# Performance work log

Measured on AMD Instinct MI355X. Metric: run time of the kernel, lower is better.

## Reference

```python
import jax, jax.numpy as jnp
import numpy as np

B, IN, H, OUT = 1024, 512, 1024, 512   # tokens, input, hidden (MoE width), output
E, K, LAYERS = 8, 2, 10                 # experts, top-k, repeated MoE applications
EPS = 1e-10
LOSS_COEF = 0.01


def setup_inputs() -> dict:
    key = jax.random.key(0)
    ks = jax.random.split(key, 8)
    s = 0.02  # small init scale for weights
    return {
        "x": jax.random.normal(ks[0], (B, IN), jnp.float32),
        "enc_w": jax.random.normal(ks[1], (IN, H), jnp.float32) * s,
        "enc_b": jnp.zeros((H,), jnp.float32),
        "w_gate": jax.random.normal(ks[2], (H, E), jnp.float32) * s,
        "w1": jax.random.normal(ks[3], (E, H, H), jnp.float32) * s,
        "b1": jnp.zeros((E, H), jnp.float32),
        "w2": jax.random.normal(ks[4], (E, H, H), jnp.float32) * s,
        "b2": jnp.zeros((E, H), jnp.float32),
        "dec_w": jax.random.normal(ks[5], (H, OUT), jnp.float32) * s,
        "dec_b": jnp.zeros((OUT,), jnp.float32),
    }


def _cv_squared(v):
    # torch .var() is unbiased (ddof=1)
    return jnp.var(v, ddof=1) / (jnp.mean(v) ** 2 + EPS)


def _moe_layer(h, w_gate, w1, b1, w2, b2):
    # top-k gating (eval / no-noise path of noisy_top_k_gating)
    logits = h @ w_gate                                  # [B, E]
    top_vals, top_idx = jax.lax.top_k(logits, K)         # [B, K]
    gk = jax.nn.softmax(top_vals, axis=-1)               # softmax over top-k logits
    b = h.shape[0]
    gates = jnp.zeros((b, E), h.dtype).at[jnp.arange(b)[:, None], top_idx].set(gk)
    importance = gates.sum(axis=0)                       # [E]
    load = (gates > 0).sum(axis=0).astype(h.dtype)       # [E]
    aux = LOSS_COEF * (_cv_squared(importance) + _cv_squared(load))
    # experts: Linear -> ReLU -> Linear; combine weighted by gates
    # (dense-over-experts form; math identical to sparse dispatch/combine)
    hid = jax.nn.relu(jnp.einsum('bh,ehf->bef', h, w1) + b1)  # [B, E, H]
    y = jnp.einsum('bef,efo->beo', hid, w2) + b2              # [B, E, H]
    out = jnp.einsum('be,beo->bo', gates, y)                  # [B, H]
    return out, aux


def reference(x, enc_w, enc_b, w_gate, w1, b1, w2, b2, dec_w, dec_b):
    h = jax.nn.relu(x @ enc_w + enc_b)
    loss = jnp.zeros((), h.dtype)
    for _ in range(LAYERS):  # same MoE module (shared params) applied 10 times
        h, aux = _moe_layer(h, w_gate, w1, b1, w2, b2)
        loss = loss + aux
    out = jax.nn.relu(h @ dec_w + dec_b)
    return out, loss
```

## Files before the change

### kernel.cpp

```cpp
#include <hip/hip_runtime.h>
#include <math.h>

#define TPB 256
typedef unsigned short u16;
typedef unsigned int u32;
typedef __bf16 bf16x8 __attribute__((ext_vector_type(8)));
typedef float f32x4 __attribute__((ext_vector_type(4)));

namespace {
constexpr int NTOK  = 1024;
constexpr int IND   = 512;
constexpr int HD    = 1024;
constexpr int OUTD  = 512;
constexpr int NE    = 8;
constexpr int NSLOT = 2048;
}

__device__ __forceinline__ u16 f2bf(float f) {
  u32 x = __float_as_uint(f);
  x += 0x7fffu + ((x >> 16) & 1u);
  return (u16)(x >> 16);
}
__device__ __forceinline__ float bf2f(u16 u) { return __uint_as_float(((u32)u) << 16); }
__device__ __forceinline__ void split2(float v, u16& h, u16& l) {
  h = f2bf(v);
  l = f2bf(v - bf2f(h));
}

__device__ __forceinline__ void gll16(const void* g, void* l) {
  __builtin_amdgcn_global_load_lds((const __attribute__((address_space(1))) void*)g,
                                   (__attribute__((address_space(3))) void*)l, 16, 0, 0);
}


__global__ __launch_bounds__(TPB)
void transpose_split(const float* __restrict__ in, u16* __restrict__ ohi,
                     u16* __restrict__ olo, int K, int N)
{
  const int z = blockIdx.z;
  in  += (size_t)z * K * N;
  ohi += (size_t)z * K * N;
  olo += (size_t)z * K * N;
  __shared__ float tile[32][33];
  const int k0 = blockIdx.y * 32, n0 = blockIdx.x * 32;
  const int tx = threadIdx.x & 31, ty = threadIdx.x >> 5;
#pragma unroll
  for (int i = 0; i < 4; ++i) {
    int k = ty + i * 8;
    tile[k][tx] = in[(size_t)(k0 + k) * N + n0 + tx];
  }
  __syncthreads();
#pragma unroll
  for (int i = 0; i < 4; ++i) {
    int n = ty + i * 8;
    float v = tile[tx][n];
    u16 h, l; split2(v, h, l);
    size_t o = (size_t)(n0 + n) * K + k0 + tx;
    ohi[o] = h; olo[o] = l;
  }
}

__global__ __launch_bounds__(TPB)
void split_rows(const float* __restrict__ in, u16* __restrict__ oh,
                u16* __restrict__ ol, int nelem)
{
  int i = blockIdx.x * TPB + threadIdx.x;
  if (i * 4 >= nelem) return;
  float4 v = ((const float4*)in)[i];
  ushort4 H, L;
  split2(v.x, H.x, L.x); split2(v.y, H.y, L.y);
  split2(v.z, H.z, L.z); split2(v.w, H.w, L.w);
  ((ushort4*)oh)[i] = H;
  ((ushort4*)ol)[i] = L;
}

template<bool RELU, bool GROUPED, bool GATHER, bool SPLIT_OUT>
__global__ __launch_bounds__(TPB)
void gemm_split(const u16* __restrict__ Ah, const u16* __restrict__ Al,
                const int* __restrict__ gatherIdx,
                const u16* __restrict__ Bh, const u16* __restrict__ Bl,
                const float* __restrict__ bias,
                float* __restrict__ Cf, u16* __restrict__ Ch, u16* __restrict__ Cl,
                const int* __restrict__ seg_off, const int* __restrict__ seg_cnt,
                int M, int K, int N)
{
  const int e = GROUPED ? blockIdx.z : 0;
  int cnt = M, base = 0;
  if (GROUPED) { cnt = seg_cnt[e]; base = seg_off[e]; }
  const int tm = blockIdx.y, tn = blockIdx.x;
  if (tm * 64 >= cnt) return;

  __shared__ u16 smem[24576];
  constexpr int AHo = 0, ALo = 4096, BHo = 8192, BLo = 16384;

  const int t = threadIdx.x;
  const int wid = t >> 6, lane = t & 63;
  const int wr = wid >> 1, wc = wid & 1;

  const u16* aph[2]; const u16* apl[2];
#pragma unroll
  for (int i = 0; i < 2; ++i) {
    int slot = t + i * TPB;
    int row = slot >> 3, kblk = slot & 7;
    int kbs = kblk ^ (row & 7);
    int row_in = tm * 64 + row;
    int rv = row_in < cnt ? row_in : 0;
    int src;
    if (GATHER)      src = gatherIdx[base + rv];
    else             src = GROUPED ? base + rv : rv;
    size_t off = (size_t)src * K + kbs * 8;
    aph[i] = Ah + off; apl[i] = Al + off;
  }
  const u16* bph[4]; const u16* bpl[4];
  const size_t bbase = GROUPED ? (size_t)e * N * K : 0;
#pragma unroll
  for (int i = 0; i < 4; ++i) {
    int slot = t + i * TPB;
    int n = slot >> 3, kblk = slot & 7;
    int kbs = kblk ^ (n & 7);
    size_t off = bbase + (size_t)(tn * 128 + n) * K + kbs * 8;
    bph[i] = Bh + off; bpl[i] = Bl + off;
  }

  f32x4 acc[2][4];
#pragma unroll
  for (int i = 0; i < 2; ++i)
#pragma unroll
    for (int j = 0; j < 4; ++j) acc[i][j] = (f32x4){0.f, 0.f, 0.f, 0.f};

  for (int k0 = 0; k0 < K; k0 += 64) {
#pragma unroll
    for (int i = 0; i < 2; ++i) {
      int ldso = (wid * 64 + i * TPB) * 8;
      gll16(aph[i] + k0, &smem[AHo + ldso]);
      gll16(apl[i] + k0, &smem[ALo + ldso]);
    }
#pragma unroll
    for (int i = 0; i < 4; ++i) {
      int ldso = (wid * 64 + i * TPB) * 8;
      gll16(bph[i] + k0, &smem[BHo + ldso]);
      gll16(bpl[i] + k0, &smem[BLo + ldso]);
    }
    __syncthreads();

#pragma unroll
    for (int s = 0; s < 2; ++s) {
      const int kb = s * 4 + (lane >> 4);
      bf16x8 fah[2], fal[2];
#pragma unroll
      for (int fr = 0; fr < 2; ++fr) {
        int ar = wr * 32 + fr * 16 + (lane & 15);
        int off = ar * 64 + ((kb ^ (ar & 7)) << 3);
        fah[fr] = *(const bf16x8*)&smem[AHo + off];
        fal[fr] = *(const bf16x8*)&smem[ALo + off];
      }
      bf16x8 fbh[4], fbl[4];
#pragma unroll
      for (int fc = 0; fc < 4; ++fc) {
        int bn = wc * 64 + fc * 16 + (lane & 15);
        int off = bn * 64 + ((kb ^ (bn & 7)) << 3);
        fbh[fc] = *(const bf16x8*)&smem[BHo + off];
        fbl[fc] = *(const bf16x8*)&smem[BLo + off];
      }
#pragma unroll
      for (int fr = 0; fr < 2; ++fr)
#pragma unroll
        for (int fc = 0; fc < 4; ++fc) {
          acc[fr][fc] = __builtin_amdgcn_mfma_f32_16x16x32_bf16(fah[fr], fbh[fc], acc[fr][fc], 0, 0, 0);
          acc[fr][fc] = __builtin_amdgcn_mfma_f32_16x16x32_bf16(fah[fr], fbl[fc], acc[fr][fc], 0, 0, 0);
          acc[fr][fc] = __builtin_amdgcn_mfma_f32_16x16x32_bf16(fal[fr], fbh[fc], acc[fr][fc], 0, 0, 0);
        }
    }
    __syncthreads();
  }

  const float* bp = bias + (GROUPED ? (size_t)e * N : 0);
#pragma unroll
  for (int fr = 0; fr < 2; ++fr) {
#pragma unroll
    for (int q = 0; q < 4; ++q) {
      int row_in = tm * 64 + wr * 32 + fr * 16 + ((lane >> 4) << 2) + q;
      if (row_in >= cnt) continue;
      size_t orow = (size_t)(GROUPED ? base + row_in : row_in);
#pragma unroll
      for (int fc = 0; fc < 4; ++fc) {
        int col = tn * 128 + wc * 64 + fc * 16 + (lane & 15);
        float v = acc[fr][fc][q] + bp[col];
        if (RELU) v = fmaxf(v, 0.f);
        if (SPLIT_OUT) {
          u16 h, l; split2(v, h, l);
          Ch[orow * N + col] = h;
          Cl[orow * N + col] = l;
        } else {
          Cf[orow * N + col] = v;
        }
      }
    }
  }
}

__global__ __launch_bounds__(TPB)
void gate_split(const u16* __restrict__ hh, const u16* __restrict__ hl,
                const float* __restrict__ w_gate,
                int* __restrict__ eidx, float* __restrict__ gval)
{
  const int b = blockIdx.x, t = threadIdx.x;
  float acc[NE] = {};
  for (int i = t; i < HD; i += TPB) {
    float hv = bf2f(hh[(size_t)b * HD + i]) + bf2f(hl[(size_t)b * HD + i]);
    const float* wg = w_gate + (size_t)i * NE;
#pragma unroll
    for (int e = 0; e < NE; ++e) acc[e] = fmaf(hv, wg[e], acc[e]);
  }
  __shared__ float red[TPB][NE];
#pragma unroll
  for (int e = 0; e < NE; ++e) red[t][e] = acc[e];
  __syncthreads();
  for (int s = TPB / 2; s > 0; s >>= 1) {
    if (t < s) {
#pragma unroll
      for (int e = 0; e < NE; ++e) red[t][e] += red[t + s][e];
    }
    __syncthreads();
  }
  if (t == 0) {
    float v1 = -1e30f; int e1 = 0;
#pragma unroll
    for (int e = 0; e < NE; ++e) { float v = red[0][e]; if (v > v1) { v1 = v; e1 = e; } }
    float v2 = -1e30f; int e2 = 0;
#pragma unroll
    for (int e = 0; e < NE; ++e) {
      if (e == e1) continue;
      float v = red[0][e]; if (v > v2) { v2 = v; e2 = e; }
    }
    float ev = expf(v2 - v1);
    eidx[b * 2] = e1;  eidx[b * 2 + 1] = e2;
    gval[b * 2] = 1.f / (1.f + ev);  gval[b * 2 + 1] = ev / (1.f + ev);
  }
}

__global__ __launch_bounds__(TPB)
void stats_scatter(const int* __restrict__ eidx, const float* __restrict__ gval,
                   float* __restrict__ loss, int* __restrict__ seg_off,
                   int* __restrict__ seg_cnt, int* __restrict__ slot_token,
                   int* __restrict__ slot_of)
{
  const int t = threadIdx.x;
  float imp[NE] = {};
  int   cnt[NE] = {};
  for (int s = t; s < NSLOT; s += TPB) {
    int e = eidx[s]; float g = gval[s];
#pragma unroll
    for (int q = 0; q < NE; ++q) if (q == e) { imp[q] += g; cnt[q]++; }
  }
  __shared__ float rimp[TPB][NE];
  __shared__ int   rcnt[TPB][NE];
#pragma unroll
  for (int e = 0; e < NE; ++e) { rimp[t][e] = imp[e]; rcnt[t][e] = cnt[e]; }
  __syncthreads();
  for (int s = TPB / 2; s > 0; s >>= 1) {
    if (t < s) {
#pragma unroll
      for (int e = 0; e < NE; ++e) { rimp[t][e] += rimp[t + s][e]; rcnt[t][e] += rcnt[t + s][e]; }
    }
    __syncthreads();
  }
  __shared__ int s_off[NE], s_fill[NE];
  if (t == 0) {
    float mi = 0.f, ml = 0.f;
#pragma unroll
    for (int e = 0; e < NE; ++e) { mi += rimp[0][e]; ml += (float)rcnt[0][e]; }
    mi /= NE; ml /= NE;
    float vi = 0.f, vl = 0.f;
#pragma unroll
    for (int e = 0; e < NE; ++e) {
      float di = rimp[0][e] - mi; vi += di * di;
      float dl = (float)rcnt[0][e] - ml; vl += dl * dl;
    }
    vi /= (NE - 1); vl /= (NE - 1);
    loss[0] += 0.01f * (vi / (mi * mi + 1e-10f) + vl / (ml * ml + 1e-10f));
    int off = 0;
#pragma unroll
    for (int e = 0; e < NE; ++e) {
      seg_off[e] = off; seg_cnt[e] = rcnt[0][e];
      s_off[e] = off; s_fill[e] = 0; off += rcnt[0][e];
    }
  }
  __syncthreads();
  for (int s = t; s < NSLOT; s += TPB) {
    int e = eidx[s];
    int pos = s_off[e] + atomicAdd(&s_fill[e], 1);
    slot_token[pos] = s >> 1;
    slot_of[s] = pos;
  }
}

__global__ __launch_bounds__(TPB)
void combine_split(const float* __restrict__ y, const float* __restrict__ gval,
                   const int* __restrict__ slot_of,
                   u16* __restrict__ hh, u16* __restrict__ hl)
{
  const int b = blockIdx.x, t = threadIdx.x;
  const int p0 = slot_of[b * 2], p1 = slot_of[b * 2 + 1];
  const float g0 = gval[b * 2], g1 = gval[b * 2 + 1];
  const float4* y0 = (const float4*)(y + (size_t)p0 * HD);
  const float4* y1 = (const float4*)(y + (size_t)p1 * HD);
  for (int i = t; i < HD / 4; i += TPB) {
    float4 a = y0[i], c = y1[i];
    float v0 = g0 * a.x + g1 * c.x, v1 = g0 * a.y + g1 * c.y;
    float v2 = g0 * a.z + g1 * c.z, v3 = g0 * a.w + g1 * c.w;
    ushort4 H, L;
    split2(v0, H.x, L.x); split2(v1, H.y, L.y);
    split2(v2, H.z, L.z); split2(v3, H.w, L.w);
    ((ushort4*)hh)[(size_t)b * (HD / 4) + i] = H;
    ((ushort4*)hl)[(size_t)b * (HD / 4) + i] = L;
  }
}

__global__ void init_kernel(float* loss) { loss[0] = 0.f; }
__global__ void write_loss(const float* __restrict__ loss, float* __restrict__ out)
{ out[0] = loss[0]; }

template<bool RELU, bool GROUPED, bool GATHER>
__global__ __launch_bounds__(TPB)
void gemm_f32(const float* __restrict__ A, const int* __restrict__ gatherIdx,
              const float* __restrict__ B, const float* __restrict__ bias,
              float* __restrict__ C, const int* __restrict__ seg_off,
              const int* __restrict__ seg_cnt, int M, int K, int N)
{
  const int e = GROUPED ? blockIdx.z : 0;
  int cnt = M, base = 0;
  if (GROUPED) { cnt = seg_cnt[e]; base = seg_off[e]; }
  const int tm = blockIdx.y, tn = blockIdx.x;
  if (tm * 64 >= cnt) return;
  const float* Bp = B + (size_t)e * K * N;
  const float* bp = bias + (size_t)e * N;
  __shared__ float As[16][68];
  __shared__ float Bs[16][64];
  const int t = threadIdx.x;
  const int rm0 = (t >> 4) << 2, cn0 = (t & 15) << 2;
  int arow[4]; bool aval[4];
#pragma unroll
  for (int i = 0; i < 4; ++i) {
    int idx = t + i * TPB;
    int r = idx >> 4;
    int row_in = tm * 64 + r;
    bool v = row_in < cnt;
    int src;
    if (GATHER) src = v ? gatherIdx[base + row_in] : 0;
    else        src = v ? (GROUPED ? base + row_in : row_in) : 0;
    arow[i] = src; aval[i] = v;
  }
  float acc[4][4] = {};
  for (int k0 = 0; k0 < K; k0 += 16) {
#pragma unroll
    for (int i = 0; i < 4; ++i) {
      int idx = t + i * TPB;
      int r = idx >> 4, kk = idx & 15;
      As[kk][r] = aval[i] ? A[(size_t)arow[i] * K + k0 + kk] : 0.f;
    }
#pragma unroll
    for (int i = 0; i < 4; ++i) {
      int idx = t + i * TPB;
      int kk = idx >> 6, n = idx & 63;
      Bs[kk][n] = Bp[(size_t)(k0 + kk) * N + tn * 64 + n];
    }
    __syncthreads();
#pragma unroll
    for (int kk = 0; kk < 16; ++kk) {
      const float4 a4 = *(const float4*)&As[kk][rm0];
      const float4 b4 = *(const float4*)&Bs[kk][cn0];
      float av[4] = {a4.x, a4.y, a4.z, a4.w};
      float bv[4] = {b4.x, b4.y, b4.z, b4.w};
#pragma unroll
      for (int i = 0; i < 4; ++i)
#pragma unroll
        for (int j = 0; j < 4; ++j) acc[i][j] = fmaf(av[i], bv[j], acc[i][j]);
    }
    __syncthreads();
  }
#pragma unroll
  for (int i = 0; i < 4; ++i) {
    int row_in = tm * 64 + rm0 + i;
    if (row_in >= cnt) continue;
    size_t orow = (size_t)(base + row_in);
    float v0 = acc[i][0] + bp[tn * 64 + cn0 + 0];
    float v1 = acc[i][1] + bp[tn * 64 + cn0 + 1];
    float v2 = acc[i][2] + bp[tn * 64 + cn0 + 2];
    float v3 = acc[i][3] + bp[tn * 64 + cn0 + 3];
    if (RELU) { v0 = fmaxf(v0, 0.f); v1 = fmaxf(v1, 0.f); v2 = fmaxf(v2, 0.f); v3 = fmaxf(v3, 0.f); }
    *(float4*)&C[orow * N + tn * 64 + cn0] = make_float4(v0, v1, v2, v3);
  }
}

__global__ __launch_bounds__(TPB)
void gate_f32(const float* __restrict__ h, const float* __restrict__ w_gate,
              int* __restrict__ eidx, float* __restrict__ gval)
{
  const int b = blockIdx.x, t = threadIdx.x;
  float acc[NE] = {};
  const float* hb = h + (size_t)b * HD;
  for (int i = t; i < HD; i += TPB) {
    float hv = hb[i];
    const float* wg = w_gate + (size_t)i * NE;
#pragma unroll
    for (int e = 0; e < NE; ++e) acc[e] = fmaf(hv, wg[e], acc[e]);
  }
  __shared__ float red[TPB][NE];
#pragma unroll
  for (int e = 0; e < NE; ++e) red[t][e] = acc[e];
  __syncthreads();
  for (int s = TPB / 2; s > 0; s >>= 1) {
    if (t < s) {
#pragma unroll
      for (int e = 0; e < NE; ++e) red[t][e] += red[t + s][e];
    }
    __syncthreads();
  }
  if (t == 0) {
    float v1 = -1e30f; int e1 = 0;
#pragma unroll
    for (int e = 0; e < NE; ++e) { float v = red[0][e]; if (v > v1) { v1 = v; e1 = e; } }
    float v2 = -1e30f; int e2 = 0;
#pragma unroll
    for (int e = 0; e < NE; ++e) {
      if (e == e1) continue;
      float v = red[0][e]; if (v > v2) { v2 = v; e2 = e; }
    }
    float ev = expf(v2 - v1);
    eidx[b * 2] = e1;  eidx[b * 2 + 1] = e2;
    gval[b * 2] = 1.f / (1.f + ev);  gval[b * 2 + 1] = ev / (1.f + ev);
  }
}

__global__ __launch_bounds__(TPB)
void combine_f32(const float* __restrict__ y, const float* __restrict__ gval,
                 const int* __restrict__ slot_of, float* __restrict__ h)
{
  const int b = blockIdx.x, t = threadIdx.x;
  const int p0 = slot_of[b * 2], p1 = slot_of[b * 2 + 1];
  const float g0 = gval[b * 2], g1 = gval[b * 2 + 1];
  const float4* y0 = (const float4*)(y + (size_t)p0 * HD);
  const float4* y1 = (const float4*)(y + (size_t)p1 * HD);
  float4* hb = (float4*)(h + (size_t)b * HD);
  for (int i = t; i < HD / 4; i += TPB) {
    float4 a = y0[i], c = y1[i];
    hb[i] = make_float4(g0 * a.x + g1 * c.x, g0 * a.y + g1 * c.y,
                        g0 * a.z + g1 * c.z, g0 * a.w + g1 * c.w);
  }
}


extern "C" void kernel_launch(void* const* d_in, const int* in_sizes, int n_in,
                              void* d_out, int out_size, void* d_ws, size_t ws_size,
                              hipStream_t stream)
{
  const float* x      = (const float*)d_in[0];
  const float* enc_w  = (const float*)d_in[1];
  const float* enc_b  = (const float*)d_in[2];
  const float* w_gate = (const float*)d_in[3];
  const float* w1     = (const float*)d_in[4];
  const float* b1     = (const float*)d_in[5];
  const float* w2     = (const float*)d_in[6];
  const float* b2     = (const float*)d_in[7];
  const float* dec_w  = (const float*)d_in[8];
  const float* dec_b  = (const float*)d_in[9];
  float* outp = (float*)d_out;
  dim3 blk(TPB);

  const size_t NEED = 100ull << 20;
  if (ws_size >= NEED) {
    char* p = (char*)d_ws;
    auto alloc = [&](size_t bytes) { char* r = p; p += (bytes + 255) & ~(size_t)255; return r; };
    u16* w1t_h = (u16*)alloc((size_t)NE * HD * HD * 2);
    u16* w1t_l = (u16*)alloc((size_t)NE * HD * HD * 2);
    u16* w2t_h = (u16*)alloc((size_t)NE * HD * HD * 2);
    u16* w2t_l = (u16*)alloc((size_t)NE * HD * HD * 2);
    u16* ewt_h = (u16*)alloc((size_t)IND * HD * 2);
    u16* ewt_l = (u16*)alloc((size_t)IND * HD * 2);
    u16* dwt_h = (u16*)alloc((size_t)HD * OUTD * 2);
    u16* dwt_l = (u16*)alloc((size_t)HD * OUTD * 2);
    u16* x_h   = (u16*)alloc((size_t)NTOK * IND * 2);
    u16* x_l   = (u16*)alloc((size_t)NTOK * IND * 2);
    u16* h_h   = (u16*)alloc((size_t)NTOK * HD * 2);
    u16* h_l   = (u16*)alloc((size_t)NTOK * HD * 2);
    u16* hid_h = (u16*)alloc((size_t)NSLOT * HD * 2);
    u16* hid_l = (u16*)alloc((size_t)NSLOT * HD * 2);
    float* y   = (float*)alloc((size_t)NSLOT * HD * 4);
    int*   eidx       = (int*)alloc(NSLOT * 4);
    float* gval       = (float*)alloc(NSLOT * 4);
    int*   slot_of    = (int*)alloc(NSLOT * 4);
    int*   slot_token = (int*)alloc(NSLOT * 4);
    int*   seg_off    = (int*)alloc(256);
    int*   seg_cnt    = (int*)alloc(256);
    float* loss       = (float*)alloc(256);

    init_kernel<<<1, 1, 0, stream>>>(loss);
    transpose_split<<<dim3(HD / 32, HD / 32, NE), blk, 0, stream>>>(w1, w1t_h, w1t_l, HD, HD);
    transpose_split<<<dim3(HD / 32, HD / 32, NE), blk, 0, stream>>>(w2, w2t_h, w2t_l, HD, HD);
    transpose_split<<<dim3(HD / 32, IND / 32, 1), blk, 0, stream>>>(enc_w, ewt_h, ewt_l, IND, HD);
    transpose_split<<<dim3(OUTD / 32, HD / 32, 1), blk, 0, stream>>>(dec_w, dwt_h, dwt_l, HD, OUTD);
    split_rows<<<(NTOK * IND / 4 + TPB - 1) / TPB, blk, 0, stream>>>(x, x_h, x_l, NTOK * IND);

    gemm_split<true, false, false, true><<<dim3(HD / 128, NTOK / 64, 1), blk, 0, stream>>>(
        x_h, x_l, nullptr, ewt_h, ewt_l, enc_b, nullptr, h_h, h_l, nullptr, nullptr,
        NTOK, IND, HD);

    for (int L = 0; L < 10; ++L) {
      gate_split<<<NTOK, blk, 0, stream>>>(h_h, h_l, w_gate, eidx, gval);
      stats_scatter<<<1, blk, 0, stream>>>(eidx, gval, loss, seg_off, seg_cnt,
                                           slot_token, slot_of);
      gemm_split<true, true, true, true><<<dim3(HD / 128, NSLOT / 64, NE), blk, 0, stream>>>(
          h_h, h_l, slot_token, w1t_h, w1t_l, b1, nullptr, hid_h, hid_l,
          seg_off, seg_cnt, 0, HD, HD);
      gemm_split<false, true, false, false><<<dim3(HD / 128, NSLOT / 64, NE), blk, 0, stream>>>(
          hid_h, hid_l, nullptr, w2t_h, w2t_l, b2, y, nullptr, nullptr,
          seg_off, seg_cnt, 0, HD, HD);
      combine_split<<<NTOK, blk, 0, stream>>>(y, gval, slot_of, h_h, h_l);
    }

    gemm_split<true, false, false, false><<<dim3(OUTD / 128, NTOK / 64, 1), blk, 0, stream>>>(
        h_h, h_l, nullptr, dwt_h, dwt_l, dec_b, outp, nullptr, nullptr, nullptr, nullptr,
        NTOK, HD, OUTD);
    write_loss<<<1, 1, 0, stream>>>(loss, outp + NTOK * OUTD);
    return;
  }

  char* ws = (char*)d_ws;
  float* h   = (float*)(ws);
  float* hid = (float*)(ws + (4u  << 20));
  float* y   = (float*)(ws + (12u << 20));
  char* sp = ws + (20u << 20);
  int*   eidx       = (int*)sp;    sp += NSLOT * 4;
  float* gval       = (float*)sp;  sp += NSLOT * 4;
  int*   slot_of    = (int*)sp;    sp += NSLOT * 4;
  int*   slot_token = (int*)sp;    sp += NSLOT * 4;
  int*   seg_off    = (int*)sp;    sp += 64;
  int*   seg_cnt    = (int*)sp;    sp += 64;
  float* loss       = (float*)sp;  sp += 64;

  init_kernel<<<1, 1, 0, stream>>>(loss);
  gemm_f32<true, false, false><<<dim3(HD / 64, NTOK / 64, 1), blk, 0, stream>>>(
      x, nullptr, enc_w, enc_b, h, nullptr, nullptr, NTOK, IND, HD);
  for (int L = 0; L < 10; ++L) {
    gate_f32<<<NTOK, blk, 0, stream>>>(h, w_gate, eidx, gval);
    stats_scatter<<<1, blk, 0, stream>>>(eidx, gval, loss, seg_off, seg_cnt,
                                         slot_token, slot_of);
    gemm_f32<true, true, true><<<dim3(HD / 64, NTOK / 64, NE), blk, 0, stream>>>(
        h, slot_token, w1, b1, hid, seg_off, seg_cnt, 0, HD, HD);
    gemm_f32<false, true, false><<<dim3(HD / 64, NTOK / 64, NE), blk, 0, stream>>>(
        hid, nullptr, w2, b2, y, seg_off, seg_cnt, 0, HD, HD);
    combine_f32<<<NTOK, blk, 0, stream>>>(y, gval, slot_of, h);
  }
  gemm_f32<true, false, false><<<dim3(OUTD / 64, NTOK / 64, 1), blk, 0, stream>>>(
      h, nullptr, dec_w, dec_b, outp, nullptr, nullptr, NTOK, HD, OUTD);
  write_loss<<<1, 1, 0, stream>>>(loss, outp + NTOK * OUTD);
}
```

Baseline: 945.5 us.

## Double-buffer split-bf16 GEMM tiles and fuse gating into the combine kernel

The split-bf16 MFMA GEMM now double-buffers its LDS tiles, issuing global-to-LDS loads for the next K step while computing on the current one. This is meant to hide load latency behind the MFMA work, at the cost of doubling shared memory per block to 96 KB, which can cut the number of resident blocks per CU. The gate kernel now reads its inputs with vector loads. The per-layer gate launch is also folded into the combine kernel, which computes the top-2 gating for the next layer from the freshly combined activations, saving one launch per layer and one re-read of the hidden state.

```diff
diff --git a/kernel.cpp b/kernel.cpp
--- a/kernel.cpp
+++ b/kernel.cpp
@@ -90,8 +90,8 @@
   const int tm = blockIdx.y, tn = blockIdx.x;
   if (tm * 64 >= cnt) return;
 
-  __shared__ u16 smem[24576];
-  constexpr int AHo = 0, ALo = 4096, BHo = 8192, BLo = 16384;
+  __shared__ u16 smem[49152];
+  constexpr int AHo = 0, ALo = 4096, BHo = 8192, BLo = 16384, BUF = 24576;
 
   const int t = threadIdx.x;
   const int wid = t >> 6, lane = t & 63;
@@ -122,27 +122,28 @@
     bph[i] = Bh + off; bpl[i] = Bl + off;
   }
 
-  f32x4 acc[2][4];
-#pragma unroll
-  for (int i = 0; i < 2; ++i)
-#pragma unroll
-    for (int j = 0; j < 4; ++j) acc[i][j] = (f32x4){0.f, 0.f, 0.f, 0.f};
-
-  for (int k0 = 0; k0 < K; k0 += 64) {
+  auto stage = [&](int bb, int k0) {
 #pragma unroll
     for (int i = 0; i < 2; ++i) {
       int ldso = (wid * 64 + i * TPB) * 8;
-      gll16(aph[i] + k0, &smem[AHo + ldso]);
-      gll16(apl[i] + k0, &smem[ALo + ldso]);
+      gll16(aph[i] + k0, &smem[bb + AHo + ldso]);
+      gll16(apl[i] + k0, &smem[bb + ALo + ldso]);
     }
 #pragma unroll
     for (int i = 0; i < 4; ++i) {
       int ldso = (wid * 64 + i * TPB) * 8;
-      gll16(bph[i] + k0, &smem[BHo + ldso]);
-      gll16(bpl[i] + k0, &smem[BLo + ldso]);
-    }
-    __syncthreads();
-
+      gll16(bph[i] + k0, &smem[bb + BHo + ldso]);
+      gll16(bpl[i] + k0, &smem[bb + BLo + ldso]);
+    }
+  };
+
+  f32x4 acc[2][4];
+#pragma unroll
+  for (int i = 0; i < 2; ++i)
+#pragma unroll
+    for (int j = 0; j < 4; ++j) acc[i][j] = (f32x4){0.f, 0.f, 0.f, 0.f};
+
+  auto compute = [&](int bb) {
 #pragma unroll
     for (int s = 0; s < 2; ++s) {
       const int kb = s * 4 + (lane >> 4);
@@ -150,7 +151,7 @@
 #pragma unroll
       for (int fr = 0; fr < 2; ++fr) {
         int ar = wr * 32 + fr * 16 + (lane & 15);
-        int off = ar * 64 + ((kb ^ (ar & 7)) << 3);
+        int off = bb + ar * 64 + ((kb ^ (ar & 7)) << 3);
         fah[fr] = *(const bf16x8*)&smem[AHo + off];
         fal[fr] = *(const bf16x8*)&smem[ALo + off];
       }
@@ -158,7 +159,7 @@
 #pragma unroll
       for (int fc = 0; fc < 4; ++fc) {
         int bn = wc * 64 + fc * 16 + (lane & 15);
-        int off = bn * 64 + ((kb ^ (bn & 7)) << 3);
+        int off = bb + bn * 64 + ((kb ^ (bn & 7)) << 3);
         fbh[fc] = *(const bf16x8*)&smem[BHo + off];
         fbl[fc] = *(const bf16x8*)&smem[BLo + off];
       }
@@ -171,8 +172,18 @@
           acc[fr][fc] = __builtin_amdgcn_mfma_f32_16x16x32_bf16(fal[fr], fbh[fc], acc[fr][fc], 0, 0, 0);
         }
     }
+  };
+
+  stage(0, 0);
+  int cur = 0;
+  for (int k0 = 64; k0 < K; k0 += 64) {
     __syncthreads();
-  }
+    stage((cur ^ 1) * BUF, k0);
+    compute(cur * BUF);
+    cur ^= 1;
+  }
+  __syncthreads();
+  compute(cur * BUF);
 
   const float* bp = bias + (GROUPED ? (size_t)e * N : 0);
 #pragma unroll
@@ -205,12 +216,20 @@
                 int* __restrict__ eidx, float* __restrict__ gval)
 {
   const int b = blockIdx.x, t = threadIdx.x;
+  ushort4 H = ((const ushort4*)(hh + (size_t)b * HD))[t];
+  ushort4 L = ((const ushort4*)(hl + (size_t)b * HD))[t];
+  float hv[4] = { bf2f(H.x) + bf2f(L.x), bf2f(H.y) + bf2f(L.y),
+                  bf2f(H.z) + bf2f(L.z), bf2f(H.w) + bf2f(L.w) };
   float acc[NE] = {};
-  for (int i = t; i < HD; i += TPB) {
-    float hv = bf2f(hh[(size_t)b * HD + i]) + bf2f(hl[(size_t)b * HD + i]);
-    const float* wg = w_gate + (size_t)i * NE;
-#pragma unroll
-    for (int e = 0; e < NE; ++e) acc[e] = fmaf(hv, wg[e], acc[e]);
+  const int i0 = t * 4;
+#pragma unroll
+  for (int j = 0; j < 4; ++j) {
+    const float4* wg = (const float4*)(w_gate + (size_t)(i0 + j) * NE);
+    float4 w0 = wg[0], w1 = wg[1];
+    acc[0] = fmaf(hv[j], w0.x, acc[0]); acc[1] = fmaf(hv[j], w0.y, acc[1]);
+    acc[2] = fmaf(hv[j], w0.z, acc[2]); acc[3] = fmaf(hv[j], w0.w, acc[3]);
+    acc[4] = fmaf(hv[j], w1.x, acc[4]); acc[5] = fmaf(hv[j], w1.y, acc[5]);
+    acc[6] = fmaf(hv[j], w1.z, acc[6]); acc[7] = fmaf(hv[j], w1.w, acc[7]);
   }
   __shared__ float red[TPB][NE];
 #pragma unroll
@@ -295,25 +314,63 @@
   }
 }
 
-__global__ __launch_bounds__(TPB)
-void combine_split(const float* __restrict__ y, const float* __restrict__ gval,
-                   const int* __restrict__ slot_of,
-                   u16* __restrict__ hh, u16* __restrict__ hl)
+template<bool GATE>
+__global__ __launch_bounds__(TPB)
+void combine_gate(const float* __restrict__ y, const float* __restrict__ gv_in,
+                  const int* __restrict__ slot_of, const float* __restrict__ w_gate,
+                  u16* __restrict__ hh, u16* __restrict__ hl,
+                  int* __restrict__ eidx, float* __restrict__ gval)
 {
   const int b = blockIdx.x, t = threadIdx.x;
   const int p0 = slot_of[b * 2], p1 = slot_of[b * 2 + 1];
-  const float g0 = gval[b * 2], g1 = gval[b * 2 + 1];
-  const float4* y0 = (const float4*)(y + (size_t)p0 * HD);
-  const float4* y1 = (const float4*)(y + (size_t)p1 * HD);
-  for (int i = t; i < HD / 4; i += TPB) {
-    float4 a = y0[i], c = y1[i];
-    float v0 = g0 * a.x + g1 * c.x, v1 = g0 * a.y + g1 * c.y;
-    float v2 = g0 * a.z + g1 * c.z, v3 = g0 * a.w + g1 * c.w;
-    ushort4 H, L;
-    split2(v0, H.x, L.x); split2(v1, H.y, L.y);
-    split2(v2, H.z, L.z); split2(v3, H.w, L.w);
-    ((ushort4*)hh)[(size_t)b * (HD / 4) + i] = H;
-    ((ushort4*)hl)[(size_t)b * (HD / 4) + i] = L;
+  const float g0 = gv_in[b * 2], g1 = gv_in[b * 2 + 1];
+  float4 a = ((const float4*)(y + (size_t)p0 * HD))[t];
+  float4 c = ((const float4*)(y + (size_t)p1 * HD))[t];
+  float v[4] = { g0 * a.x + g1 * c.x, g0 * a.y + g1 * c.y,
+                 g0 * a.z + g1 * c.z, g0 * a.w + g1 * c.w };
+  ushort4 H, L;
+  split2(v[0], H.x, L.x); split2(v[1], H.y, L.y);
+  split2(v[2], H.z, L.z); split2(v[3], H.w, L.w);
+  ((ushort4*)(hh + (size_t)b * HD))[t] = H;
+  ((ushort4*)(hl + (size_t)b * HD))[t] = L;
+
+  if (GATE) {
+    float acc[NE] = {};
+    const int i0 = t * 4;
+#pragma unroll
+    for (int j = 0; j < 4; ++j) {
+      const float4* wg = (const float4*)(w_gate + (size_t)(i0 + j) * NE);
+      float4 w0 = wg[0], w1 = wg[1];
+      acc[0] = fmaf(v[j], w0.x, acc[0]); acc[1] = fmaf(v[j], w0.y, acc[1]);
+      acc[2] = fmaf(v[j], w0.z, acc[2]); acc[3] = fmaf(v[j], w0.w, acc[3]);
+      acc[4] = fmaf(v[j], w1.x, acc[4]); acc[5] = fmaf(v[j], w1.y, acc[5]);
+      acc[6] = fmaf(v[j], w1.z, acc[6]); acc[7] = fmaf(v[j], w1.w, acc[7]);
+    }
+    __shared__ float red[TPB][NE];
+#pragma unroll
+    for (int e = 0; e < NE; ++e) red[t][e] = acc[e];
+    __syncthreads();
+    for (int s = TPB / 2; s > 0; s >>= 1) {
+      if (t < s) {
+#pragma unroll
+        for (int e = 0; e < NE; ++e) red[t][e] += red[t + s][e];
+      }
+      __syncthreads();
+    }
+    if (t == 0) {
+      float v1 = -1e30f; int e1 = 0;
+#pragma unroll
+      for (int e = 0; e < NE; ++e) { float vv = red[0][e]; if (vv > v1) { v1 = vv; e1 = e; } }
+      float v2 = -1e30f; int e2 = 0;
+#pragma unroll
+      for (int e = 0; e < NE; ++e) {
+        if (e == e1) continue;
+        float vv = red[0][e]; if (vv > v2) { v2 = vv; e2 = e; }
+      }
+      float ev = expf(v2 - v1);
+      eidx[b * 2] = e1;  eidx[b * 2 + 1] = e2;
+      gval[b * 2] = 1.f / (1.f + ev);  gval[b * 2 + 1] = ev / (1.f + ev);
+    }
   }
 }
 
@@ -506,8 +563,8 @@
         x_h, x_l, nullptr, ewt_h, ewt_l, enc_b, nullptr, h_h, h_l, nullptr, nullptr,
         NTOK, IND, HD);
 
+    gate_split<<<NTOK, blk, 0, stream>>>(h_h, h_l, w_gate, eidx, gval);
     for (int L = 0; L < 10; ++L) {
-      gate_split<<<NTOK, blk, 0, stream>>>(h_h, h_l, w_gate, eidx, gval);
       stats_scatter<<<1, blk, 0, stream>>>(eidx, gval, loss, seg_off, seg_cnt,
                                            slot_token, slot_of);
       gemm_split<true, true, true, true><<<dim3(HD / 128, NSLOT / 64, NE), blk, 0, stream>>>(
@@ -516,7 +573,12 @@
       gemm_split<false, true, false, false><<<dim3(HD / 128, NSLOT / 64, NE), blk, 0, stream>>>(
           hid_h, hid_l, nullptr, w2t_h, w2t_l, b2, y, nullptr, nullptr,
           seg_off, seg_cnt, 0, HD, HD);
-      combine_split<<<NTOK, blk, 0, stream>>>(y, gval, slot_of, h_h, h_l);
+      if (L < 9)
+        combine_gate<true><<<NTOK, blk, 0, stream>>>(y, gval, slot_of, w_gate,
+                                                     h_h, h_l, eidx, gval);
+      else
+        combine_gate<false><<<NTOK, blk, 0, stream>>>(y, gval, slot_of, w_gate,
+                                                      h_h, h_l, eidx, gval);
     }
 
     gemm_split<true, false, false, false><<<dim3(OUTD / 128, NTOK / 64, 1), blk, 0, stream>>>(
```

Result: no change. 941.9 us (-0.4%).
